# Kernel optimization log

Hardware: AMD Instinct MI355X
Metric: run time of the kernel (lower is better)

The kernel has to match this reference:

```python
import jax, jax.numpy as jnp
import numpy as np

B, T, D = 2, 4096, 512
H = 8
HD = D // H  # 64


def setup_inputs() -> dict:
    key = jax.random.key(0)
    k1, k2, k3 = jax.random.split(key, 3)
    x = jax.random.normal(k1, (B, T, D), dtype=jnp.float32)
    w_qkv = jax.random.normal(k2, (3 * D, D), dtype=jnp.float32) * (1.0 / np.sqrt(D))
    w_out = jax.random.normal(k3, (D, D), dtype=jnp.float32) * (1.0 / np.sqrt(D))
    return {"x": x, "w_qkv": w_qkv, "w_out": w_out}


def reference(x, w_qkv, w_out):
    b, t, d = x.shape
    qkv = x @ w_qkv.T                      # [B,T,3D]
    q, k, v = jnp.split(qkv, 3, axis=-1)
    # b t (h d) -> b h t d
    def split_heads(a):
        return a.reshape(b, t, H, HD).transpose(0, 2, 1, 3)
    q, k, v = split_heads(q), split_heads(k), split_heads(v)
    scale = 1.0 / np.sqrt(HD).astype(np.float32)
    scores = jnp.einsum('bhqd,bhkd->bhqk', q, k) * scale  # [B,H,T,T]
    causal = jnp.tril(jnp.ones((t, t), dtype=bool))        # keep lower triangle
    scores = jnp.where(causal[None, None], scores, -jnp.inf)
    attn = jax.nn.softmax(scores, axis=-1)
    out = jnp.einsum('bhqk,bhkd->bhqd', attn, v)           # [B,H,T,HD]
    out = out.transpose(0, 2, 1, 3).reshape(b, t, d)       # b h t d -> b t (h d)
    return out @ w_out.T
```

## Files before the change

kernel.cpp:

```cpp
#include <hip/hip_runtime.h>
#include <hip/hip_bf16.h>

#define BB 2
#define TT 4096
#define DD 512
#define HH 8
#define HD 64
#define M_TOT (BB*TT)
#define N_QKV (3*DD)

typedef __attribute__((ext_vector_type(8))) __bf16 bf16x8;
typedef __attribute__((ext_vector_type(4))) float f32x4;

#define MFMA16(a,b,c) __builtin_amdgcn_mfma_f32_16x16x32_bf16((a),(b),(c),0,0,0)

#define SCALE_L2E 0.18033688011112443f
#define SHIFT_L2E 11.541560327111707f

static __device__ __forceinline__ unsigned short f2bf(float f) {
    union { float f; unsigned u; } v; v.f = f;
    return (unsigned short)((v.u + 0x8000u) >> 16);
}
static __device__ __forceinline__ unsigned short f2bf_t(float f) {
    union { float f; unsigned u; } v; v.f = f;
    return (unsigned short)(v.u >> 16);
}

static __device__ __forceinline__ bf16x8 load8(const unsigned short* p) {
    bf16x8 v;
    __builtin_memcpy(&v, p, 16);
    return v;
}

static __device__ __forceinline__ bf16x8 ones_frag() {
    unsigned short u[8];
    #pragma unroll
    for (int i = 0; i < 8; i++) u[i] = 0x3F80;
    bf16x8 v; __builtin_memcpy(&v, u, 16);
    return v;
}

#define GLDS(gp, lp) __builtin_amdgcn_global_load_lds( \
    (const __attribute__((address_space(1))) unsigned int*)(gp), \
    (__attribute__((address_space(3))) unsigned int*)(lp), 16, 0, 0)

#define NX4 (M_TOT*DD/4)
#define NW4 (N_QKV*DD/4)
#define NO4 (DD*DD/4)
__global__ __launch_bounds__(256) void cast_all(
        const float* __restrict__ x, const float* __restrict__ wqkv,
        const float* __restrict__ wout,
        unsigned short* __restrict__ xb, unsigned short* __restrict__ wqkvb,
        unsigned short* __restrict__ woutb) {
    int i = blockIdx.x * 256 + threadIdx.x;
    const float* s; unsigned short* d; int j;
    if (i < NX4)            { s = x;    d = xb;    j = i; }
    else if (i < NX4 + NW4) { s = wqkv; d = wqkvb; j = i - NX4; }
    else                    { s = wout; d = woutb; j = i - NX4 - NW4; }
    float4 f = ((const float4*)s)[j];
    ushort4 o;
    o.x = f2bf(f.x); o.y = f2bf(f.y); o.z = f2bf(f.z); o.w = f2bf(f.w);
    ((ushort4*)d)[j] = o;
}

__global__ __launch_bounds__(256) void qkv_gemm(
        const unsigned short* __restrict__ xb,
        const unsigned short* __restrict__ wb,
        unsigned short* __restrict__ qb,
        unsigned short* __restrict__ kb,
        unsigned short* __restrict__ vtb) {
    __shared__ union {
        struct { unsigned short As[128 * 32]; unsigned short Bs[128 * 32]; } g;
        unsigned short vt[4][64][72];
    } sm;
    int tid = threadIdx.x;
    int w = tid >> 6, lane = tid & 63;
    int lrow = lane & 15, quad = lane >> 4;
    int bn = blockIdx.x % (N_QKV / 128);
    int bm = blockIdx.x / (N_QKV / 128);
    int m0 = bm * 128, n0 = bn * 128;
    int wm = w >> 1, wn = w & 1;

    f32x4 c[4][4];
    #pragma unroll
    for (int i = 0; i < 4; i++)
        #pragma unroll
        for (int j = 0; j < 4; j++) c[i][j] = (f32x4){0.f, 0.f, 0.f, 0.f};

    for (int k0 = 0; k0 < DD; k0 += 32) {
        #pragma unroll
        for (int j = 0; j < 2; j++) {
            int ch = j * 256 + tid;
            int row = ch >> 2, kc = ch & 3;
            GLDS(xb + (size_t)(m0 + row) * DD + k0 + kc * 8,
                 (char*)sm.g.As + (size_t)(j * 256 + w * 64) * 16);
        }
        #pragma unroll
        for (int j = 0; j < 2; j++) {
            int ch = j * 256 + tid;
            int row = ch >> 2, kc = ch & 3;
            GLDS(wb + (size_t)(n0 + row) * DD + k0 + kc * 8,
                 (char*)sm.g.Bs + (size_t)(j * 256 + w * 64) * 16);
        }
        __syncthreads();
        bf16x8 a[4], b[4];
        #pragma unroll
        for (int mf = 0; mf < 4; mf++) a[mf] = load8(&sm.g.As[(wm * 64 + mf * 16 + lrow) * 32 + quad * 8]);
        #pragma unroll
        for (int nf = 0; nf < 4; nf++) b[nf] = load8(&sm.g.Bs[(wn * 64 + nf * 16 + lrow) * 32 + quad * 8]);
        #pragma unroll
        for (int mf = 0; mf < 4; mf++)
            #pragma unroll
            for (int nf = 0; nf < 4; nf++)
                c[mf][nf] = MFMA16(a[mf], b[nf], c[mf][nf]);
        __syncthreads();
    }

    int m0w = m0 + wm * 64, n0w = n0 + wn * 64;
    int which = n0w >> 9;
    int h = (n0w & 511) >> 6;
    if (which < 2) {
        unsigned short* dst = (which == 0) ? qb : kb;
        #pragma unroll
        for (int mf = 0; mf < 4; mf++) {
            #pragma unroll
            for (int r = 0; r < 4; r++) {
                int m = m0w + mf * 16 + quad * 4 + r;
                int t = m & (TT - 1), bi = m >> 12;
                size_t hb = (size_t)(bi * HH + h) * TT + t;
                #pragma unroll
                for (int nf = 0; nf < 4; nf++) {
                    int d = nf * 16 + lrow;
                    dst[hb * HD + d] = f2bf(c[mf][nf][r]);
                }
            }
        }
    } else {
        #pragma unroll
        for (int mf = 0; mf < 4; mf++)
            #pragma unroll
            for (int r = 0; r < 4; r++)
                #pragma unroll
                for (int nf = 0; nf < 4; nf++)
                    sm.vt[w][nf * 16 + lrow][mf * 16 + quad * 4 + r] = f2bf(c[mf][nf][r]);
        int bi = m0w >> 12, t0 = m0w & (TT - 1);
        size_t hb = (size_t)(bi * HH + h) * HD;
        #pragma unroll
        for (int i = 0; i < 8; i++) {
            int d = i * 8 + (lane >> 3);
            int tc = (lane & 7) * 8;
            bf16x8 v;
            __builtin_memcpy(&v, &sm.vt[w][d][tc], 16);
            __builtin_memcpy(vtb + (hb + d) * TT + t0 + tc, &v, 16);
        }
    }
}

__global__ __launch_bounds__(256) void attn_kernel(
        const unsigned short* __restrict__ qb,
        const unsigned short* __restrict__ kb,
        const unsigned short* __restrict__ vtb,
        float* __restrict__ ows, float* __restrict__ lws) {
    __shared__ union {
        unsigned short p[4][64][68];
        float c[2][64][66];
    } sm;

    int w = threadIdx.x >> 6;
    int lane = threadIdx.x & 63;
    int lrow = lane & 15, quad = lane >> 4;
    int bh = blockIdx.x & 15;
    int pr = (blockIdx.x >> 4) & 31;
    int seg = blockIdx.x >> 9;

    const unsigned short* qh = qb + (size_t)bh * TT * HD;
    const unsigned short* kh = kb + (size_t)bh * TT * HD;
    const unsigned short* vth = vtb + (size_t)bh * HD * TT;
    bf16x8 ones = ones_frag();

    int kres = (seg * 4 + w + pr) & 7;

    for (int half = 0; half < 2; half++) {
        int qt = half ? (63 - pr) : pr;
        int q0 = qt * 64;

        bf16x8 qf[4][2];
        #pragma unroll
        for (int mf = 0; mf < 4; mf++) {
            const unsigned short* qp = qh + (q0 + mf * 16 + lrow) * HD + quad * 8;
            qf[mf][0] = load8(qp);
            qf[mf][1] = load8(qp + 32);
        }

        f32x4 o[4][4];
        f32x4 l[4];
        #pragma unroll
        for (int i = 0; i < 4; i++) {
            l[i] = (f32x4){0.f, 0.f, 0.f, 0.f};
            #pragma unroll
            for (int j = 0; j < 4; j++) o[i][j] = (f32x4){0.f, 0.f, 0.f, 0.f};
        }

        for (int kt = kres; kt <= qt; kt += 8) {
            int kbase = kt * 64;
            bool diag = (kt == qt);
            bf16x8 vf[4][2];
            #pragma unroll
            for (int nfd = 0; nfd < 4; nfd++) {
                const unsigned short* vp = vth + (nfd * 16 + lrow) * TT + kbase + quad * 8;
                vf[nfd][0] = load8(vp);
                vf[nfd][1] = load8(vp + 32);
            }
            #pragma unroll
            for (int nf = 0; nf < 4; nf++) {
                const unsigned short* kp = kh + (kbase + nf * 16 + lrow) * HD + quad * 8;
                bf16x8 kf0 = load8(kp);
                bf16x8 kf1 = load8(kp + 32);
                #pragma unroll
                for (int mf = 0; mf < 4; mf++) {
                    if (diag && nf > mf) {
                        #pragma unroll
                        for (int r = 0; r < 4; r++)
                            sm.p[w][mf * 16 + quad * 4 + r][nf * 16 + lrow] = 0;
                    } else {
                        f32x4 sv = {0.f, 0.f, 0.f, 0.f};
                        sv = MFMA16(qf[mf][0], kf0, sv);
                        sv = MFMA16(qf[mf][1], kf1, sv);
                        #pragma unroll
                        for (int r = 0; r < 4; r++) {
                            float p = __builtin_amdgcn_exp2f(sv[r] * SCALE_L2E - SHIFT_L2E);
                            if (diag && nf == mf && lrow > quad * 4 + r) p = 0.f;
                            sm.p[w][mf * 16 + quad * 4 + r][nf * 16 + lrow] = f2bf_t(p);
                        }
                    }
                }
            }
            #pragma unroll
            for (int mf = 0; mf < 4; mf++) {
                bf16x8 pa0, pa1;
                __builtin_memcpy(&pa0, &sm.p[w][mf * 16 + lrow][quad * 8], 16);
                __builtin_memcpy(&pa1, &sm.p[w][mf * 16 + lrow][32 + quad * 8], 16);
                l[mf] = MFMA16(pa0, ones, l[mf]);
                l[mf] = MFMA16(pa1, ones, l[mf]);
                #pragma unroll
                for (int nfd = 0; nfd < 4; nfd++) {
                    o[mf][nfd] = MFMA16(pa0, vf[nfd][0], o[mf][nfd]);
                    o[mf][nfd] = MFMA16(pa1, vf[nfd][1], o[mf][nfd]);
                }
            }
        }

        __syncthreads();
        if (w >= 2) {
            int cb = w - 2;
            #pragma unroll
            for (int mf = 0; mf < 4; mf++)
                #pragma unroll
                for (int r = 0; r < 4; r++) {
                    int row = mf * 16 + quad * 4 + r;
                    #pragma unroll
                    for (int nfd = 0; nfd < 4; nfd++)
                        sm.c[cb][row][nfd * 16 + lrow] = o[mf][nfd][r];
                    if (lrow == 0) sm.c[cb][row][64] = l[mf][r];
                }
        }
        __syncthreads();
        if (w < 2) {
            #pragma unroll
            for (int mf = 0; mf < 4; mf++)
                #pragma unroll
                for (int r = 0; r < 4; r++) {
                    int row = mf * 16 + quad * 4 + r;
                    #pragma unroll
                    for (int nfd = 0; nfd < 4; nfd++)
                        sm.c[w][row][nfd * 16 + lrow] += o[mf][nfd][r];
                    if (lrow == 0) sm.c[w][row][64] += l[mf][r];
                }
        }
        __syncthreads();
        size_t tbase = ((size_t)(bh * 64 + qt) * 2 + seg) * 64;
        #pragma unroll
        for (int r = 0; r < 4; r++) {
            int row = w * 16 + quad * 4 + r;
            if (lrow == 0)
                lws[tbase + row] = sm.c[0][row][64] + sm.c[1][row][64];
            #pragma unroll
            for (int nfd = 0; nfd < 4; nfd++) {
                int col = nfd * 16 + lrow;
                ows[(tbase + row) * 64 + col] = sm.c[0][row][col] + sm.c[1][row][col];
            }
        }
        __syncthreads();
    }
}

__global__ __launch_bounds__(256) void attn_norm(
        const float* __restrict__ ows, const float* __restrict__ lws,
        unsigned short* __restrict__ attnb) {
    int g = blockIdx.x;
    int bh = g >> 6, qt = g & 63;
    int bi = bh >> 3, h = bh & 7;
    int row = threadIdx.x >> 2, dg = threadIdx.x & 3;
    size_t r0 = ((size_t)g * 2 + 0) * 64 + row;
    size_t r1 = r0 + 64;
    float inv = 1.0f / (lws[r0] + lws[r1]);
    const float4* p0 = (const float4*)(ows + r0 * 64 + dg * 16);
    const float4* p1 = (const float4*)(ows + r1 * 64 + dg * 16);
    int t = qt * 64 + row;
    unsigned short* dst = attnb + ((size_t)(bi * TT + t)) * DD + h * HD + dg * 16;
    ushort4 outv[4];
    #pragma unroll
    for (int j = 0; j < 4; j++) {
        float4 a = p0[j], b = p1[j];
        outv[j].x = f2bf_t((a.x + b.x) * inv);
        outv[j].y = f2bf_t((a.y + b.y) * inv);
        outv[j].z = f2bf_t((a.z + b.z) * inv);
        outv[j].w = f2bf_t((a.w + b.w) * inv);
    }
    __builtin_memcpy(dst, outv, 32);
}

__global__ __launch_bounds__(256) void proj_gemm(
        const unsigned short* __restrict__ ab,
        const unsigned short* __restrict__ wb,
        float* __restrict__ out) {
    __shared__ unsigned short As[128 * 32];
    __shared__ unsigned short Bs[128 * 32];
    int tid = threadIdx.x;
    int w = tid >> 6, lane = tid & 63;
    int lrow = lane & 15, quad = lane >> 4;
    int bn = blockIdx.x % (DD / 128);
    int bm = blockIdx.x / (DD / 128);
    int m0 = bm * 128, n0 = bn * 128;
    int wm = w >> 1, wn = w & 1;

    f32x4 c[4][4];
    #pragma unroll
    for (int i = 0; i < 4; i++)
        #pragma unroll
        for (int j = 0; j < 4; j++) c[i][j] = (f32x4){0.f, 0.f, 0.f, 0.f};

    for (int k0 = 0; k0 < DD; k0 += 32) {
        #pragma unroll
        for (int j = 0; j < 2; j++) {
            int ch = j * 256 + tid;
            int row = ch >> 2, kc = ch & 3;
            GLDS(ab + (size_t)(m0 + row) * DD + k0 + kc * 8,
                 (char*)As + (size_t)(j * 256 + w * 64) * 16);
        }
        #pragma unroll
        for (int j = 0; j < 2; j++) {
            int ch = j * 256 + tid;
            int row = ch >> 2, kc = ch & 3;
            GLDS(wb + (size_t)(n0 + row) * DD + k0 + kc * 8,
                 (char*)Bs + (size_t)(j * 256 + w * 64) * 16);
        }
        __syncthreads();
        bf16x8 a[4], b[4];
        #pragma unroll
        for (int mf = 0; mf < 4; mf++) a[mf] = load8(&As[(wm * 64 + mf * 16 + lrow) * 32 + quad * 8]);
        #pragma unroll
        for (int nf = 0; nf < 4; nf++) b[nf] = load8(&Bs[(wn * 64 + nf * 16 + lrow) * 32 + quad * 8]);
        #pragma unroll
        for (int mf = 0; mf < 4; mf++)
            #pragma unroll
            for (int nf = 0; nf < 4; nf++)
                c[mf][nf] = MFMA16(a[mf], b[nf], c[mf][nf]);
        __syncthreads();
    }

    #pragma unroll
    for (int mf = 0; mf < 4; mf++) {
        #pragma unroll
        for (int r = 0; r < 4; r++) {
            int m = m0 + wm * 64 + mf * 16 + quad * 4 + r;
            #pragma unroll
            for (int nf = 0; nf < 4; nf++) {
                int n = n0 + wn * 64 + nf * 16 + lrow;
                out[(size_t)m * DD + n] = c[mf][nf][r];
            }
        }
    }
}

extern "C" void kernel_launch(void* const* d_in, const int* in_sizes, int n_in,
                              void* d_out, int out_size, void* d_ws, size_t ws_size,
                              hipStream_t stream) {
    const float* x    = (const float*)d_in[0];
    const float* wqkv = (const float*)d_in[1];
    const float* wout = (const float*)d_in[2];
    float* out = (float*)d_out;

    char* ws = (char*)d_ws;
    unsigned short* xb    = (unsigned short*)ws; ws += (size_t)M_TOT * DD * 2;
    unsigned short* wqkvb = (unsigned short*)ws; ws += (size_t)N_QKV * DD * 2;
    unsigned short* woutb = (unsigned short*)ws; ws += (size_t)DD * DD * 2;
    unsigned short* qb    = (unsigned short*)ws; ws += (size_t)BB * HH * TT * HD * 2;
    unsigned short* kb    = (unsigned short*)ws; ws += (size_t)BB * HH * TT * HD * 2;
    unsigned short* vtb   = (unsigned short*)ws; ws += (size_t)BB * HH * HD * TT * 2;
    unsigned short* attnb = (unsigned short*)ws; ws += (size_t)M_TOT * DD * 2;
    float* ows = (float*)ws; ws += (size_t)1024 * 2 * 64 * 64 * 4;
    float* lws = (float*)ws; ws += (size_t)1024 * 2 * 64 * 4;

    cast_all<<<(NX4 + NW4 + NO4) / 256, 256, 0, stream>>>(x, wqkv, wout, xb, wqkvb, woutb);

    qkv_gemm<<<(M_TOT / 128) * (N_QKV / 128), 256, 0, stream>>>(xb, wqkvb, qb, kb, vtb);

    attn_kernel<<<1024, 256, 0, stream>>>(qb, kb, vtb, ows, lws);

    attn_norm<<<1024, 256, 0, stream>>>(ows, lws, attnb);

    proj_gemm<<<(M_TOT / 128) * (DD / 128), 256, 0, stream>>>(attnb, woutb, out);
}
```

Baseline: 202.0 us.

## Keep attention P in registers via transposed MFMA and fuse normalization

```diff
diff --git a/kernel.cpp b/kernel.cpp
--- a/kernel.cpp
+++ b/kernel.cpp
@@ -10,9 +10,20 @@
 #define N_QKV (3*DD)
 
 typedef __attribute__((ext_vector_type(8))) __bf16 bf16x8;
+typedef __attribute__((ext_vector_type(4))) __bf16 bf16x4;
+typedef __attribute__((ext_vector_type(4))) short s16x4;
 typedef __attribute__((ext_vector_type(4))) float f32x4;
 
-#define MFMA16(a,b,c) __builtin_amdgcn_mfma_f32_16x16x32_bf16((a),(b),(c),0,0,0)
+#define MFMA32(a,b,c) __builtin_amdgcn_mfma_f32_16x16x32_bf16((a),(b),(c),0,0,0)
+
+static __device__ __forceinline__ f32x4 mfma_k16(s16x4 a, s16x4 b, f32x4 c) {
+#if __has_builtin(__builtin_amdgcn_mfma_f32_16x16x16_bf16)
+    return __builtin_amdgcn_mfma_f32_16x16x16_bf16(
+        __builtin_bit_cast(bf16x4, a), __builtin_bit_cast(bf16x4, b), c, 0, 0, 0);
+#else
+    return __builtin_amdgcn_mfma_f32_16x16x16bf16_1k(a, b, c, 0, 0, 0);
+#endif
+}
 
 #define SCALE_L2E 0.18033688011112443f
 #define SHIFT_L2E 11.541560327111707f
@@ -31,13 +42,18 @@
     __builtin_memcpy(&v, p, 16);
     return v;
 }
-
-static __device__ __forceinline__ bf16x8 ones_frag() {
-    unsigned short u[8];
-    #pragma unroll
-    for (int i = 0; i < 8; i++) u[i] = 0x3F80;
-    bf16x8 v; __builtin_memcpy(&v, u, 16);
+static __device__ __forceinline__ s16x4 load4(const unsigned short* p) {
+    s16x4 v;
+    __builtin_memcpy(&v, p, 8);
     return v;
+}
+static __device__ __forceinline__ s16x4 pack4(float a, float b, float c, float d) {
+    union { unsigned u[2]; s16x4 v; } r;
+    union { float f; unsigned u; } x0, x1, x2, x3;
+    x0.f = a; x1.f = b; x2.f = c; x3.f = d;
+    r.u[0] = (x0.u >> 16) | (x1.u & 0xffff0000u);
+    r.u[1] = (x2.u >> 16) | (x3.u & 0xffff0000u);
+    return r.v;
 }
 
 #define GLDS(gp, lp) __builtin_amdgcn_global_load_lds( \
@@ -112,7 +128,7 @@
         for (int mf = 0; mf < 4; mf++)
             #pragma unroll
             for (int nf = 0; nf < 4; nf++)
-                c[mf][nf] = MFMA16(a[mf], b[nf], c[mf][nf]);
+                c[mf][nf] = MFMA32(a[mf], b[nf], c[mf][nf]);
         __syncthreads();
     }
 
@@ -129,10 +145,8 @@
                 int t = m & (TT - 1), bi = m >> 12;
                 size_t hb = (size_t)(bi * HH + h) * TT + t;
                 #pragma unroll
-                for (int nf = 0; nf < 4; nf++) {
-                    int d = nf * 16 + lrow;
-                    dst[hb * HD + d] = f2bf(c[mf][nf][r]);
-                }
+                for (int nf = 0; nf < 4; nf++)
+                    dst[hb * HD + nf * 16 + lrow] = f2bf(c[mf][nf][r]);
             }
         }
     } else {
@@ -160,164 +174,152 @@
         const unsigned short* __restrict__ qb,
         const unsigned short* __restrict__ kb,
         const unsigned short* __restrict__ vtb,
-        float* __restrict__ ows, float* __restrict__ lws) {
-    __shared__ union {
-        unsigned short p[4][64][68];
-        float c[2][64][66];
-    } sm;
-
+        unsigned short* __restrict__ attnb) {
+    __shared__ float cbuf[2 * 64 * 66];
+
+    const f32x4 ZERO4 = {0.f, 0.f, 0.f, 0.f};
     int w = threadIdx.x >> 6;
     int lane = threadIdx.x & 63;
     int lrow = lane & 15, quad = lane >> 4;
     int bh = blockIdx.x & 15;
-    int pr = (blockIdx.x >> 4) & 31;
-    int seg = blockIdx.x >> 9;
+    int pr = blockIdx.x >> 4;
+    int bi = bh >> 3, h = bh & 7;
 
     const unsigned short* qh = qb + (size_t)bh * TT * HD;
     const unsigned short* kh = kb + (size_t)bh * TT * HD;
     const unsigned short* vth = vtb + (size_t)bh * HD * TT;
-    bf16x8 ones = ones_frag();
-
-    int kres = (seg * 4 + w + pr) & 7;
 
     for (int half = 0; half < 2; half++) {
         int qt = half ? (63 - pr) : pr;
         int q0 = qt * 64;
 
-        bf16x8 qf[4][2];
-        #pragma unroll
-        for (int mf = 0; mf < 4; mf++) {
-            const unsigned short* qp = qh + (q0 + mf * 16 + lrow) * HD + quad * 8;
-            qf[mf][0] = load8(qp);
-            qf[mf][1] = load8(qp + 32);
+        bf16x8 qB[4][2];
+        #pragma unroll
+        for (int qf = 0; qf < 4; qf++) {
+            const unsigned short* qp = qh + (q0 + qf * 16 + lrow) * HD + quad * 8;
+            qB[qf][0] = load8(qp);
+            qB[qf][1] = load8(qp + 32);
         }
 
         f32x4 o[4][4];
-        f32x4 l[4];
-        #pragma unroll
-        for (int i = 0; i < 4; i++) {
-            l[i] = (f32x4){0.f, 0.f, 0.f, 0.f};
-            #pragma unroll
-            for (int j = 0; j < 4; j++) o[i][j] = (f32x4){0.f, 0.f, 0.f, 0.f};
-        }
-
-        for (int kt = kres; kt <= qt; kt += 8) {
+        float ladd[4] = {0.f, 0.f, 0.f, 0.f};
+        #pragma unroll
+        for (int i = 0; i < 4; i++)
+            #pragma unroll
+            for (int j = 0; j < 4; j++) o[i][j] = ZERO4;
+
+        for (int kt = w; kt <= qt; kt += 4) {
             int kbase = kt * 64;
-            bool diag = (kt == qt);
-            bf16x8 vf[4][2];
-            #pragma unroll
-            for (int nfd = 0; nfd < 4; nfd++) {
-                const unsigned short* vp = vth + (nfd * 16 + lrow) * TT + kbase + quad * 8;
-                vf[nfd][0] = load8(vp);
-                vf[nfd][1] = load8(vp + 32);
-            }
-            #pragma unroll
-            for (int nf = 0; nf < 4; nf++) {
-                const unsigned short* kp = kh + (kbase + nf * 16 + lrow) * HD + quad * 8;
-                bf16x8 kf0 = load8(kp);
-                bf16x8 kf1 = load8(kp + 32);
-                #pragma unroll
-                for (int mf = 0; mf < 4; mf++) {
-                    if (diag && nf > mf) {
+            if (kt < qt) {
+                #pragma unroll
+                for (int tf = 0; tf < 4; tf++) {
+                    const unsigned short* kp = kh + (kbase + tf * 16 + lrow) * HD + quad * 8;
+                    bf16x8 kf0 = load8(kp);
+                    bf16x8 kf1 = load8(kp + 32);
+                    s16x4 vfr[4];
+                    #pragma unroll
+                    for (int df = 0; df < 4; df++)
+                        vfr[df] = load4(vth + (df * 16 + lrow) * TT + kbase + tf * 16 + quad * 4);
+                    #pragma unroll
+                    for (int qf = 0; qf < 4; qf++) {
+                        f32x4 s = MFMA32(kf0, qB[qf][0], ZERO4);
+                        s = MFMA32(kf1, qB[qf][1], s);
+                        float p0 = __builtin_amdgcn_exp2f(s[0] * SCALE_L2E - SHIFT_L2E);
+                        float p1 = __builtin_amdgcn_exp2f(s[1] * SCALE_L2E - SHIFT_L2E);
+                        float p2 = __builtin_amdgcn_exp2f(s[2] * SCALE_L2E - SHIFT_L2E);
+                        float p3 = __builtin_amdgcn_exp2f(s[3] * SCALE_L2E - SHIFT_L2E);
+                        ladd[qf] += (p0 + p1) + (p2 + p3);
+                        s16x4 pf = pack4(p0, p1, p2, p3);
                         #pragma unroll
-                        for (int r = 0; r < 4; r++)
-                            sm.p[w][mf * 16 + quad * 4 + r][nf * 16 + lrow] = 0;
-                    } else {
-                        f32x4 sv = {0.f, 0.f, 0.f, 0.f};
-                        sv = MFMA16(qf[mf][0], kf0, sv);
-                        sv = MFMA16(qf[mf][1], kf1, sv);
+                        for (int df = 0; df < 4; df++)
+                            o[df][qf] = mfma_k16(vfr[df], pf, o[df][qf]);
+                    }
+                }
+            } else {
+                #pragma unroll
+                for (int tf = 0; tf < 4; tf++) {
+                    const unsigned short* kp = kh + (kbase + tf * 16 + lrow) * HD + quad * 8;
+                    bf16x8 kf0 = load8(kp);
+                    bf16x8 kf1 = load8(kp + 32);
+                    s16x4 vfr[4];
+                    #pragma unroll
+                    for (int df = 0; df < 4; df++)
+                        vfr[df] = load4(vth + (df * 16 + lrow) * TT + kbase + tf * 16 + quad * 4);
+                    #pragma unroll
+                    for (int qf = 0; qf < 4; qf++) {
+                        if (qf < tf) continue;
+                        f32x4 s = MFMA32(kf0, qB[qf][0], ZERO4);
+                        s = MFMA32(kf1, qB[qf][1], s);
+                        float p[4];
                         #pragma unroll
                         for (int r = 0; r < 4; r++) {
-                            float p = __builtin_amdgcn_exp2f(sv[r] * SCALE_L2E - SHIFT_L2E);
-                            if (diag && nf == mf && lrow > quad * 4 + r) p = 0.f;
-                            sm.p[w][mf * 16 + quad * 4 + r][nf * 16 + lrow] = f2bf_t(p);
+                            p[r] = __builtin_amdgcn_exp2f(s[r] * SCALE_L2E - SHIFT_L2E);
+                            if (qf == tf && quad * 4 + r > lrow) p[r] = 0.f;
                         }
+                        ladd[qf] += (p[0] + p[1]) + (p[2] + p[3]);
+                        s16x4 pf = pack4(p[0], p[1], p[2], p[3]);
+                        #pragma unroll
+                        for (int df = 0; df < 4; df++)
+                            o[df][qf] = mfma_k16(vfr[df], pf, o[df][qf]);
                     }
                 }
             }
-            #pragma unroll
-            for (int mf = 0; mf < 4; mf++) {
-                bf16x8 pa0, pa1;
-                __builtin_memcpy(&pa0, &sm.p[w][mf * 16 + lrow][quad * 8], 16);
-                __builtin_memcpy(&pa1, &sm.p[w][mf * 16 + lrow][32 + quad * 8], 16);
-                l[mf] = MFMA16(pa0, ones, l[mf]);
-                l[mf] = MFMA16(pa1, ones, l[mf]);
-                #pragma unroll
-                for (int nfd = 0; nfd < 4; nfd++) {
-                    o[mf][nfd] = MFMA16(pa0, vf[nfd][0], o[mf][nfd]);
-                    o[mf][nfd] = MFMA16(pa1, vf[nfd][1], o[mf][nfd]);
-                }
-            }
+        }
+
+        #pragma unroll
+        for (int qf = 0; qf < 4; qf++) {
+            ladd[qf] += __shfl_xor(ladd[qf], 16);
+            ladd[qf] += __shfl_xor(ladd[qf], 32);
         }
 
         __syncthreads();
         if (w >= 2) {
             int cb = w - 2;
             #pragma unroll
-            for (int mf = 0; mf < 4; mf++)
-                #pragma unroll
-                for (int r = 0; r < 4; r++) {
-                    int row = mf * 16 + quad * 4 + r;
-                    #pragma unroll
-                    for (int nfd = 0; nfd < 4; nfd++)
-                        sm.c[cb][row][nfd * 16 + lrow] = o[mf][nfd][r];
-                    if (lrow == 0) sm.c[cb][row][64] = l[mf][r];
-                }
+            for (int df = 0; df < 4; df++)
+                #pragma unroll
+                for (int qf = 0; qf < 4; qf++)
+                    #pragma unroll
+                    for (int r = 0; r < 4; r++)
+                        cbuf[(cb * 64 + qf * 16 + lrow) * 66 + df * 16 + quad * 4 + r] = o[df][qf][r];
+            if (quad == 0)
+                #pragma unroll
+                for (int qf = 0; qf < 4; qf++)
+                    cbuf[(cb * 64 + qf * 16 + lrow) * 66 + 64] = ladd[qf];
         }
         __syncthreads();
         if (w < 2) {
             #pragma unroll
-            for (int mf = 0; mf < 4; mf++)
-                #pragma unroll
-                for (int r = 0; r < 4; r++) {
-                    int row = mf * 16 + quad * 4 + r;
-                    #pragma unroll
-                    for (int nfd = 0; nfd < 4; nfd++)
-                        sm.c[w][row][nfd * 16 + lrow] += o[mf][nfd][r];
-                    if (lrow == 0) sm.c[w][row][64] += l[mf][r];
-                }
-        }
-        __syncthreads();
-        size_t tbase = ((size_t)(bh * 64 + qt) * 2 + seg) * 64;
-        #pragma unroll
-        for (int r = 0; r < 4; r++) {
-            int row = w * 16 + quad * 4 + r;
-            if (lrow == 0)
-                lws[tbase + row] = sm.c[0][row][64] + sm.c[1][row][64];
-            #pragma unroll
-            for (int nfd = 0; nfd < 4; nfd++) {
-                int col = nfd * 16 + lrow;
-                ows[(tbase + row) * 64 + col] = sm.c[0][row][col] + sm.c[1][row][col];
+            for (int df = 0; df < 4; df++)
+                #pragma unroll
+                for (int qf = 0; qf < 4; qf++)
+                    #pragma unroll
+                    for (int r = 0; r < 4; r++)
+                        cbuf[(w * 64 + qf * 16 + lrow) * 66 + df * 16 + quad * 4 + r] += o[df][qf][r];
+            if (quad == 0)
+                #pragma unroll
+                for (int qf = 0; qf < 4; qf++)
+                    cbuf[(w * 64 + qf * 16 + lrow) * 66 + 64] += ladd[qf];
+        }
+        __syncthreads();
+        {
+            int q = threadIdx.x >> 2, dseg = (threadIdx.x & 3) * 16;
+            const float* r0 = &cbuf[q * 66];
+            const float* r1 = &cbuf[(64 + q) * 66];
+            float inv = 1.0f / (r0[64] + r1[64]);
+            unsigned outp[8];
+            #pragma unroll
+            for (int i = 0; i < 8; i++) {
+                float a0 = (r0[dseg + 2 * i] + r1[dseg + 2 * i]) * inv;
+                float a1 = (r0[dseg + 2 * i + 1] + r1[dseg + 2 * i + 1]) * inv;
+                outp[i] = (unsigned)f2bf_t(a0) | ((unsigned)f2bf_t(a1) << 16);
             }
+            unsigned short* dst = attnb + ((size_t)(bi * TT + q0 + q)) * DD + h * HD + dseg;
+            __builtin_memcpy(dst, outp, 16);
+            __builtin_memcpy(dst + 8, outp + 4, 16);
         }
         __syncthreads();
     }
-}
-
-__global__ __launch_bounds__(256) void attn_norm(
-        const float* __restrict__ ows, const float* __restrict__ lws,
-        unsigned short* __restrict__ attnb) {
-    int g = blockIdx.x;
-    int bh = g >> 6, qt = g & 63;
-    int bi = bh >> 3, h = bh & 7;
-    int row = threadIdx.x >> 2, dg = threadIdx.x & 3;
-    size_t r0 = ((size_t)g * 2 + 0) * 64 + row;
-    size_t r1 = r0 + 64;
-    float inv = 1.0f / (lws[r0] + lws[r1]);
-    const float4* p0 = (const float4*)(ows + r0 * 64 + dg * 16);
-    const float4* p1 = (const float4*)(ows + r1 * 64 + dg * 16);
-    int t = qt * 64 + row;
-    unsigned short* dst = attnb + ((size_t)(bi * TT + t)) * DD + h * HD + dg * 16;
-    ushort4 outv[4];
-    #pragma unroll
-    for (int j = 0; j < 4; j++) {
-        float4 a = p0[j], b = p1[j];
-        outv[j].x = f2bf_t((a.x + b.x) * inv);
-        outv[j].y = f2bf_t((a.y + b.y) * inv);
-        outv[j].z = f2bf_t((a.z + b.z) * inv);
-        outv[j].w = f2bf_t((a.w + b.w) * inv);
-    }
-    __builtin_memcpy(dst, outv, 32);
 }
 
 __global__ __launch_bounds__(256) void proj_gemm(
@@ -365,7 +367,7 @@
         for (int mf = 0; mf < 4; mf++)
             #pragma unroll
             for (int nf = 0; nf < 4; nf++)
-                c[mf][nf] = MFMA16(a[mf], b[nf], c[mf][nf]);
+                c[mf][nf] = MFMA32(a[mf], b[nf], c[mf][nf]);
         __syncthreads();
     }
 
@@ -399,16 +401,12 @@
     unsigned short* kb    = (unsigned short*)ws; ws += (size_t)BB * HH * TT * HD * 2;
     unsigned short* vtb   = (unsigned short*)ws; ws += (size_t)BB * HH * HD * TT * 2;
     unsigned short* attnb = (unsigned short*)ws; ws += (size_t)M_TOT * DD * 2;
-    float* ows = (float*)ws; ws += (size_t)1024 * 2 * 64 * 64 * 4;
-    float* lws = (float*)ws; ws += (size_t)1024 * 2 * 64 * 4;
 
     cast_all<<<(NX4 + NW4 + NO4) / 256, 256, 0, stream>>>(x, wqkv, wout, xb, wqkvb, woutb);
 
     qkv_gemm<<<(M_TOT / 128) * (N_QKV / 128), 256, 0, stream>>>(xb, wqkvb, qb, kb, vtb);
 
-    attn_kernel<<<1024, 256, 0, stream>>>(qb, kb, vtb, ows, lws);
-
-    attn_norm<<<1024, 256, 0, stream>>>(ows, lws, attnb);
+    attn_kernel<<<512, 256, 0, stream>>>(qb, kb, vtb, attnb);
 
     proj_gemm<<<(M_TOT / 128) * (DD / 128), 256, 0, stream>>>(attnb, woutb, out);
 }
```

Result: slower. 217.4 us (+7.6%).
